# Kernel tuning notes

Hardware: AMD Instinct MI355X
Metric: run time of the kernel (lower is better)

Reference implementation:

```python
import jax, jax.numpy as jnp
import numpy as np

INPUT_SIZE = 1024
HEAD_SIZE = 64


def setup_inputs() -> dict:
    key = jax.random.key(0)
    kx, kk, kq, kv = jax.random.split(key, 4)
    B, T, C, H = 4, 4096, INPUT_SIZE, HEAD_SIZE
    x = jax.random.normal(kx, (B, T, C), dtype=jnp.float32)
    # nn.Linear(C, H, bias=False) weight is (H, C); we store transposed (C, H)
    # so that y = x @ W matches torch's x @ weight.T
    scale = 1.0 / np.sqrt(C)
    Wk = jax.random.uniform(kk, (C, H), dtype=jnp.float32, minval=-scale, maxval=scale)
    Wq = jax.random.uniform(kq, (C, H), dtype=jnp.float32, minval=-scale, maxval=scale)
    Wv = jax.random.uniform(kv, (C, H), dtype=jnp.float32, minval=-scale, maxval=scale)
    return {"x": x, "Wk": Wk, "Wq": Wq, "Wv": Wv}


def reference(x, Wk, Wq, Wv):
    B, T, C = x.shape
    k = x @ Wk  # (B, T, H)
    q = x @ Wq
    v = x @ Wv
    H = k.shape[-1]
    # scaled scores (B, T, T)
    wei = jnp.einsum('bth,bsh->bts', q, k) * (H ** -0.5)
    causal = jnp.tril(jnp.ones((T, T), dtype=bool))
    wei = jnp.where(causal, wei, -jnp.inf)
    wei = jax.nn.softmax(wei, axis=-1)
    out = jnp.einsum('bts,bsh->bth', wei, v)  # (B, T, H)
    return out
```

## Files before the change

kernel.cpp:

```cpp
#include <hip/hip_runtime.h>
#include <math.h>


#define BT   16384
#define TDIM 4096
#define CDIM 1024
#define HDIM 64
#define ACCW 68
#define NSLOT 288

typedef __attribute__((ext_vector_type(8))) short bf16x8;
typedef __attribute__((ext_vector_type(4))) float f32x4;
typedef __attribute__((ext_vector_type(8))) unsigned short us8;
typedef __attribute__((ext_vector_type(4))) unsigned short us4;

static __device__ __forceinline__ unsigned short f2bf(float f) {
    unsigned int u = __float_as_uint(f);
    u += 0x7fffu + ((u >> 16) & 1u);
    return (unsigned short)(u >> 16);
}

static __device__ __forceinline__ void pswap(unsigned &x, unsigned &y) {
    asm("v_permlane32_swap_b32 %0, %1" : "+v"(x), "+v"(y));
    asm("v_permlane16_swap_b32 %0, %1" : "+v"(x), "+v"(y));
}

static __device__ __forceinline__ void softmax_pack(
    const f32x4 sT[4], bool diag, int qloc, int quad,
    bf16x8 &pa0, bf16x8 &pa1)
{
    float p[4][4];
    if (diag) {
        #pragma unroll
        for (int st = 0; st < 4; st++)
            #pragma unroll
            for (int r = 0; r < 4; r++) {
                int kkloc = st * 16 + quad * 4 + r;
                p[st][r] = (kkloc > qloc) ? 0.f : __expf(sT[st][r]);
            }
    } else {
        #pragma unroll
        for (int st = 0; st < 4; st++)
            #pragma unroll
            for (int r = 0; r < 4; r++)
                p[st][r] = __expf(sT[st][r]);
    }
    unsigned cpk[4][2];
    #pragma unroll
    for (int st = 0; st < 4; st++) {
        asm("v_cvt_pk_bf16_f32 %0, %1, %2"
            : "=v"(cpk[st][0]) : "v"(p[st][0]), "v"(p[st][1]));
        asm("v_cvt_pk_bf16_f32 %0, %1, %2"
            : "=v"(cpk[st][1]) : "v"(p[st][2]), "v"(p[st][3]));
    }
    union { unsigned u[4]; bf16x8 v; } u0, u1;
    unsigned a0 = cpk[0][0], b0 = cpk[1][0]; pswap(a0, b0);
    unsigned a1 = cpk[0][1], b1 = cpk[1][1]; pswap(a1, b1);
    u0.u[0] = a0; u0.u[1] = a1; u0.u[2] = b0; u0.u[3] = b1;
    unsigned a2 = cpk[2][0], b2 = cpk[3][0]; pswap(a2, b2);
    unsigned a3 = cpk[2][1], b3 = cpk[3][1]; pswap(a3, b3);
    u1.u[0] = a2; u1.u[1] = a3; u1.u[2] = b2; u1.u[3] = b3;
    pa0 = u0.v; pa1 = u1.v;
}

__global__ __launch_bounds__(256) void wtrans(
    const float* __restrict__ Wk, const float* __restrict__ Wq,
    const float* __restrict__ Wv, unsigned short* __restrict__ wtg)
{
    int idx = blockIdx.x * 256 + threadIdx.x;
    int mat = idx >> 16;
    int rem = idx & 65535;
    int h = rem >> 10, c = rem & 1023;
    const float* W = (mat == 0) ? Wk : (mat == 1) ? Wq : Wv;
    wtg[idx] = f2bf(W[c * HDIM + h]);
}

__global__ __launch_bounds__(512) void qkv_proj(
    const float* __restrict__ x, const unsigned short* __restrict__ wtg,
    unsigned short* __restrict__ kg, unsigned short* __restrict__ qg,
    unsigned short* __restrict__ vtg)
{
    __shared__ __align__(16) unsigned short xs[2][32][72];
    __shared__ __align__(16) unsigned short wts[2][192][72];
    const int t = threadIdx.x;
    const int lane = t & 63, wv = t >> 6, quad = lane >> 4, l16 = lane & 15;
    const int mt = wv >> 2;
    const int nq = wv & 3;
    const int row0 = blockIdx.x * 32;

    const int xr = t >> 4, xc4 = (t & 15) * 4;
    const int wn = t >> 3, wc8 = (t & 7) * 8;

    f32x4 acc3[3];
    #pragma unroll
    for (int i = 0; i < 3; i++) acc3[i] = (f32x4){0.f, 0.f, 0.f, 0.f};

    const size_t xrow = (size_t)(row0 + xr) * CDIM + xc4;

    float4 xq[8];
    #pragma unroll
    for (int c = 0; c < 8; c++)
        xq[c] = *(const float4*)&x[xrow + c * 64];

    us8 w0 = *(const us8*)&wtg[(size_t)(wn +   0) * CDIM + wc8];
    us8 w1 = *(const us8*)&wtg[(size_t)(wn +  64) * CDIM + wc8];
    us8 w2 = *(const us8*)&wtg[(size_t)(wn + 128) * CDIM + wc8];

    {
        us4 pk = { f2bf(xq[0].x), f2bf(xq[0].y), f2bf(xq[0].z), f2bf(xq[0].w) };
        *(us4*)&xs[0][xr][xc4] = pk;
        *(us8*)&wts[0][wn +   0][wc8] = w0;
        *(us8*)&wts[0][wn +  64][wc8] = w1;
        *(us8*)&wts[0][wn + 128][wc8] = w2;
    }
    xq[0] = *(const float4*)&x[xrow + 8 * 64];
    w0 = *(const us8*)&wtg[(size_t)(wn +   0) * CDIM + 64 + wc8];
    w1 = *(const us8*)&wtg[(size_t)(wn +  64) * CDIM + 64 + wc8];
    w2 = *(const us8*)&wtg[(size_t)(wn + 128) * CDIM + 64 + wc8];
    __syncthreads();

    #pragma unroll
    for (int it = 0; it < 16; it++) {
        const int buf = it & 1;
        if (it + 1 < 16) {
            const int sl = (it + 1) & 7;
            us4 pk = { f2bf(xq[sl].x), f2bf(xq[sl].y),
                       f2bf(xq[sl].z), f2bf(xq[sl].w) };
            *(us4*)&xs[buf ^ 1][xr][xc4] = pk;
            *(us8*)&wts[buf ^ 1][wn +   0][wc8] = w0;
            *(us8*)&wts[buf ^ 1][wn +  64][wc8] = w1;
            *(us8*)&wts[buf ^ 1][wn + 128][wc8] = w2;
            if (it + 9 < 16)
                xq[sl] = *(const float4*)&x[xrow + (it + 9) * 64];
            if (it + 2 < 16) {
                int nc = (it + 2) * 64;
                w0 = *(const us8*)&wtg[(size_t)(wn +   0) * CDIM + nc + wc8];
                w1 = *(const us8*)&wtg[(size_t)(wn +  64) * CDIM + nc + wc8];
                w2 = *(const us8*)&wtg[(size_t)(wn + 128) * CDIM + nc + wc8];
            }
        }
        bf16x8 a0 = *(const bf16x8*)&xs[buf][mt * 16 + l16][quad * 8];
        bf16x8 a1 = *(const bf16x8*)&xs[buf][mt * 16 + l16][32 + quad * 8];
        #pragma unroll
        for (int j = 0; j < 3; j++) {
            int nt = nq * 3 + j;
            bf16x8 b0 = *(const bf16x8*)&wts[buf][nt * 16 + l16][quad * 8];
            bf16x8 b1 = *(const bf16x8*)&wts[buf][nt * 16 + l16][32 + quad * 8];
            acc3[j] = __builtin_amdgcn_mfma_f32_16x16x32_bf16(a0, b0, acc3[j], 0, 0, 0);
            acc3[j] = __builtin_amdgcn_mfma_f32_16x16x32_bf16(a1, b1, acc3[j], 0, 0, 0);
        }
        __syncthreads();
    }

    const int mrow = row0 + mt * 16 + quad * 4;
    #pragma unroll
    for (int j = 0; j < 3; j++) {
        int nt = nq * 3 + j;
        int mat = nt >> 2;
        int col = (nt & 3) * 16 + l16;
        if (mat == 2) {
            int bb = mrow >> 12, tr = mrow & 4095;
            us4 pv = { f2bf(acc3[j][0]), f2bf(acc3[j][1]),
                       f2bf(acc3[j][2]), f2bf(acc3[j][3]) };
            *(us4*)&vtg[((size_t)(bb * HDIM + col) << 12) + tr] = pv;
        } else {
            float s = (mat == 1) ? 0.125f : 1.0f;
            unsigned short* dst = (mat == 0) ? kg : qg;
            #pragma unroll
            for (int reg = 0; reg < 4; reg++)
                dst[(size_t)(mrow + reg) * HDIM + col] = f2bf(acc3[j][reg] * s);
        }
    }
}

__global__ __launch_bounds__(256) void attn(
    const unsigned short* __restrict__ qg, const unsigned short* __restrict__ kg,
    const unsigned short* __restrict__ vtg, float* __restrict__ slabs)
{
    __shared__ __align__(16) unsigned short Ks[2][64][72];
    __shared__ __align__(16) unsigned short Vt[2][64][72];

    const int t = threadIdx.x;
    const int lane = t & 63, wv = t >> 6, quad = lane >> 4, l16 = lane & 15;

    const int b = blockIdx.x / NSLOT;
    const int s = blockIdx.x - b * NSLOT;
    int a;
    if      (s < 8)   a = 0;
    else if (s < 24)  a = 1;
    else if (s < 48)  a = 2;
    else if (s < 80)  a = 3;
    else if (s < 120) a = 4;
    else if (s < 168) a = 5;
    else if (s < 224) a = 6;
    else              a = 7;
    const int u  = s - 4 * a * (a + 1);
    const int qt = a * 8 + u / (a + 1);
    const int c  = u % (a + 1);

    const size_t bbase = (size_t)b * TDIM;
    const int Q0 = qt * 64;
    const int kt0 = c * 8;
    const int kt1 = (kt0 + 7 < qt) ? kt0 + 7 : qt;

    const int qrow = Q0 + wv * 16 + l16;
    const bf16x8 qa0 = *(const bf16x8*)&qg[(bbase + qrow) * HDIM + quad * 8];
    const bf16x8 qa1 = *(const bf16x8*)&qg[(bbase + qrow) * HDIM + 32 + quad * 8];

    const short onev = (l16 == 0) ? (short)0x3F80 : (short)0;
    const bf16x8 ones = { onev, onev, onev, onev, onev, onev, onev, onev };

    f32x4 O[5];
    #pragma unroll
    for (int i = 0; i < 5; i++) O[i] = (f32x4){0.f, 0.f, 0.f, 0.f};

    const int fr = t >> 3, fc = (t & 7) * 8;

    us8 kr0 = *(const us8*)&kg[(bbase + kt0 * 64 + fr) * HDIM + fc];
    us8 kr1 = *(const us8*)&kg[(bbase + kt0 * 64 + fr + 32) * HDIM + fc];
    us8 vr0 = *(const us8*)&vtg[((size_t)(b * HDIM + fr) << 12) + kt0 * 64 + fc];
    us8 vr1 = *(const us8*)&vtg[((size_t)(b * HDIM + fr + 32) << 12) + kt0 * 64 + fc];
    *(us8*)&Ks[0][fr][fc] = kr0;
    *(us8*)&Ks[0][fr + 32][fc] = kr1;
    *(us8*)&Vt[0][fr][fc] = vr0;
    *(us8*)&Vt[0][fr + 32][fc] = vr1;
    if (kt0 < kt1) {
        int kn = kt0 + 1;
        kr0 = *(const us8*)&kg[(bbase + kn * 64 + fr) * HDIM + fc];
        kr1 = *(const us8*)&kg[(bbase + kn * 64 + fr + 32) * HDIM + fc];
        vr0 = *(const us8*)&vtg[((size_t)(b * HDIM + fr) << 12) + kn * 64 + fc];
        vr1 = *(const us8*)&vtg[((size_t)(b * HDIM + fr + 32) << 12) + kn * 64 + fc];
    }
    __syncthreads();

    const int qloc = wv * 16 + l16;

    bf16x8 pa0, pa1;
    {
        f32x4 sT[4];
        #pragma unroll
        for (int st = 0; st < 4; st++) {
            bf16x8 kb0 = *(const bf16x8*)&Ks[0][st * 16 + l16][quad * 8];
            bf16x8 kb1 = *(const bf16x8*)&Ks[0][st * 16 + l16][32 + quad * 8];
            f32x4 z = (f32x4){0.f, 0.f, 0.f, 0.f};
            z = __builtin_amdgcn_mfma_f32_16x16x32_bf16(kb0, qa0, z, 0, 0, 0);
            z = __builtin_amdgcn_mfma_f32_16x16x32_bf16(kb1, qa1, z, 0, 0, 0);
            sT[st] = z;
        }
        softmax_pack(sT, kt0 == qt, qloc, quad, pa0, pa1);
    }

    int buf = 0;
    for (int kt = kt0; kt < kt1; ++kt) {
        *(us8*)&Ks[buf ^ 1][fr][fc] = kr0;
        *(us8*)&Ks[buf ^ 1][fr + 32][fc] = kr1;
        *(us8*)&Vt[buf ^ 1][fr][fc] = vr0;
        *(us8*)&Vt[buf ^ 1][fr + 32][fc] = vr1;
        if (kt + 2 <= kt1) {
            int kn = kt + 2;
            kr0 = *(const us8*)&kg[(bbase + kn * 64 + fr) * HDIM + fc];
            kr1 = *(const us8*)&kg[(bbase + kn * 64 + fr + 32) * HDIM + fc];
            vr0 = *(const us8*)&vtg[((size_t)(b * HDIM + fr) << 12) + kn * 64 + fc];
            vr1 = *(const us8*)&vtg[((size_t)(b * HDIM + fr + 32) << 12) + kn * 64 + fc];
        }
        __syncthreads();

        __builtin_amdgcn_s_setprio(1);
        f32x4 sT[4];
        #pragma unroll
        for (int st = 0; st < 4; st++) {
            bf16x8 kb0 = *(const bf16x8*)&Ks[buf ^ 1][st * 16 + l16][quad * 8];
            bf16x8 kb1 = *(const bf16x8*)&Ks[buf ^ 1][st * 16 + l16][32 + quad * 8];
            f32x4 z = (f32x4){0.f, 0.f, 0.f, 0.f};
            z = __builtin_amdgcn_mfma_f32_16x16x32_bf16(kb0, qa0, z, 0, 0, 0);
            z = __builtin_amdgcn_mfma_f32_16x16x32_bf16(kb1, qa1, z, 0, 0, 0);
            sT[st] = z;
        }
        #pragma unroll
        for (int nt = 0; nt < 4; nt++) {
            bf16x8 vb0 = *(const bf16x8*)&Vt[buf][nt * 16 + l16][quad * 8];
            bf16x8 vb1 = *(const bf16x8*)&Vt[buf][nt * 16 + l16][32 + quad * 8];
            O[nt] = __builtin_amdgcn_mfma_f32_16x16x32_bf16(pa0, vb0, O[nt], 0, 0, 0);
            O[nt] = __builtin_amdgcn_mfma_f32_16x16x32_bf16(pa1, vb1, O[nt], 0, 0, 0);
        }
        O[4] = __builtin_amdgcn_mfma_f32_16x16x32_bf16(pa0, ones, O[4], 0, 0, 0);
        O[4] = __builtin_amdgcn_mfma_f32_16x16x32_bf16(pa1, ones, O[4], 0, 0, 0);
        __builtin_amdgcn_s_setprio(0);

        softmax_pack(sT, (kt + 1) == qt, qloc, quad, pa0, pa1);

        __syncthreads();
        buf ^= 1;
    }

    #pragma unroll
    for (int nt = 0; nt < 4; nt++) {
        bf16x8 vb0 = *(const bf16x8*)&Vt[buf][nt * 16 + l16][quad * 8];
        bf16x8 vb1 = *(const bf16x8*)&Vt[buf][nt * 16 + l16][32 + quad * 8];
        O[nt] = __builtin_amdgcn_mfma_f32_16x16x32_bf16(pa0, vb0, O[nt], 0, 0, 0);
        O[nt] = __builtin_amdgcn_mfma_f32_16x16x32_bf16(pa1, vb1, O[nt], 0, 0, 0);
    }
    O[4] = __builtin_amdgcn_mfma_f32_16x16x32_bf16(pa0, ones, O[4], 0, 0, 0);
    O[4] = __builtin_amdgcn_mfma_f32_16x16x32_bf16(pa1, ones, O[4], 0, 0, 0);

    float* slab = slabs + (size_t)(b * NSLOT + s) * 64 * ACCW;
    const int rl = wv * 16 + quad * 4;
    #pragma unroll
    for (int nt = 0; nt < 4; nt++)
        #pragma unroll
        for (int r = 0; r < 4; r++)
            slab[(size_t)(rl + r) * ACCW + nt * 16 + l16] = O[nt][r];
    if (l16 == 0) {
        #pragma unroll
        for (int r = 0; r < 4; r++)
            slab[(size_t)(rl + r) * ACCW + 64] = O[4][r];
    }
}

__global__ __launch_bounds__(256) void reduce_norm(
    const float* __restrict__ slabs, float* __restrict__ out)
{
    int idx = blockIdx.x * 256 + threadIdx.x;
    int row = idx >> 4, c4 = (idx & 15) * 4;
    int b = row >> 12, qt = (row >> 6) & 63, r64 = row & 63;
    int a = qt >> 3, nc = a + 1;
    int base = 4 * a * (a + 1) + (qt & 7) * nc;

    const float* sl = slabs + ((size_t)(b * NSLOT + base) * 64 + r64) * ACCW;
    float4 o = make_float4(0.f, 0.f, 0.f, 0.f);
    float l = 0.f;
    for (int i = 0; i < nc; i++) {
        float4 v = *(const float4*)&sl[c4];
        o.x += v.x; o.y += v.y; o.z += v.z; o.w += v.w;
        l += sl[64];
        sl += (size_t)64 * ACCW;
    }
    float inv = 1.f / l;
    *(float4*)&out[(size_t)row * HDIM + c4] =
        make_float4(o.x * inv, o.y * inv, o.z * inv, o.w * inv);
}

extern "C" void kernel_launch(void* const* d_in, const int* in_sizes, int n_in,
                              void* d_out, int out_size, void* d_ws, size_t ws_size,
                              hipStream_t stream) {
    const float* x  = (const float*)d_in[0];
    const float* Wk = (const float*)d_in[1];
    const float* Wq = (const float*)d_in[2];
    const float* Wv = (const float*)d_in[3];
    float* out = (float*)d_out;

    unsigned short* wtg = (unsigned short*)d_ws;
    unsigned short* kg  = wtg + 196608;
    unsigned short* qg  = kg + (size_t)BT * HDIM;
    unsigned short* vtg = qg + (size_t)BT * HDIM;
    float* slabs = (float*)(vtg + (size_t)4 * HDIM * TDIM);

    wtrans<<<768, 256, 0, stream>>>(Wk, Wq, Wv, wtg);
    qkv_proj<<<BT / 32, 512, 0, stream>>>(x, wtg, kg, qg, vtg);
    attn<<<4 * NSLOT, 256, 0, stream>>>(qg, kg, vtg, slabs);
    reduce_norm<<<BT * HDIM / (4 * 256), 256, 0, stream>>>(slabs, out);
}
```

Before: 138.3 us.

## Split-K the QKV projection across waves and restage attention K/V pipeline

The QKV projection now splits the K dimension of each 64-wide chunk across two wave groups, so each wave computes both 16-row M tiles and reuses one B fragment for two MFMAs. The two partial sums are reduced through shared memory before the epilogue. The attention kernel restructures its double buffering so K tiles are prefetched one step further ahead than V tiles. The K/V shared-memory stores now sit between the QK and PV MFMA phases, which removes one barrier per iteration. The aim is fewer LDS reads in the projection and better overlap of global loads with MFMA work in attention, at the cost of an extra LDS reduction and a more complex buffer-index scheme.

```diff
diff --git a/kernel.cpp b/kernel.cpp
--- a/kernel.cpp
+++ b/kernel.cpp
@@ -84,16 +84,18 @@
     __shared__ __align__(16) unsigned short wts[2][192][72];
     const int t = threadIdx.x;
     const int lane = t & 63, wv = t >> 6, quad = lane >> 4, l16 = lane & 15;
-    const int mt = wv >> 2;
+    const int kh = wv >> 2;
     const int nq = wv & 3;
     const int row0 = blockIdx.x * 32;
 
     const int xr = t >> 4, xc4 = (t & 15) * 4;
     const int wn = t >> 3, wc8 = (t & 7) * 8;
 
-    f32x4 acc3[3];
-    #pragma unroll
-    for (int i = 0; i < 3; i++) acc3[i] = (f32x4){0.f, 0.f, 0.f, 0.f};
+    f32x4 acc[2][3];
+    #pragma unroll
+    for (int m = 0; m < 2; m++)
+        #pragma unroll
+        for (int j = 0; j < 3; j++) acc[m][j] = (f32x4){0.f, 0.f, 0.f, 0.f};
 
     const size_t xrow = (size_t)(row0 + xr) * CDIM + xc4;
 
@@ -139,36 +141,59 @@
                 w2 = *(const us8*)&wtg[(size_t)(wn + 128) * CDIM + nc + wc8];
             }
         }
-        bf16x8 a0 = *(const bf16x8*)&xs[buf][mt * 16 + l16][quad * 8];
-        bf16x8 a1 = *(const bf16x8*)&xs[buf][mt * 16 + l16][32 + quad * 8];
+        bf16x8 a0 = *(const bf16x8*)&xs[buf][l16][kh * 32 + quad * 8];
+        bf16x8 a1 = *(const bf16x8*)&xs[buf][16 + l16][kh * 32 + quad * 8];
         #pragma unroll
         for (int j = 0; j < 3; j++) {
             int nt = nq * 3 + j;
-            bf16x8 b0 = *(const bf16x8*)&wts[buf][nt * 16 + l16][quad * 8];
-            bf16x8 b1 = *(const bf16x8*)&wts[buf][nt * 16 + l16][32 + quad * 8];
-            acc3[j] = __builtin_amdgcn_mfma_f32_16x16x32_bf16(a0, b0, acc3[j], 0, 0, 0);
-            acc3[j] = __builtin_amdgcn_mfma_f32_16x16x32_bf16(a1, b1, acc3[j], 0, 0, 0);
+            bf16x8 bb = *(const bf16x8*)&wts[buf][nt * 16 + l16][kh * 32 + quad * 8];
+            acc[0][j] = __builtin_amdgcn_mfma_f32_16x16x32_bf16(a0, bb, acc[0][j], 0, 0, 0);
+            acc[1][j] = __builtin_amdgcn_mfma_f32_16x16x32_bf16(a1, bb, acc[1][j], 0, 0, 0);
         }
         __syncthreads();
     }
 
-    const int mrow = row0 + mt * 16 + quad * 4;
-    #pragma unroll
-    for (int j = 0; j < 3; j++) {
-        int nt = nq * 3 + j;
-        int mat = nt >> 2;
-        int col = (nt & 3) * 16 + l16;
-        if (mat == 2) {
-            int bb = mrow >> 12, tr = mrow & 4095;
-            us4 pv = { f2bf(acc3[j][0]), f2bf(acc3[j][1]),
-                       f2bf(acc3[j][2]), f2bf(acc3[j][3]) };
-            *(us4*)&vtg[((size_t)(bb * HDIM + col) << 12) + tr] = pv;
-        } else {
-            float s = (mat == 1) ? 0.125f : 1.0f;
-            unsigned short* dst = (mat == 0) ? kg : qg;
+    float* red = (float*)&wts[0][0][0];
+    if (kh == 1) {
+        const int base = ((wv - 4) * 64 + lane) * 24;
+        #pragma unroll
+        for (int m = 0; m < 2; m++)
             #pragma unroll
-            for (int reg = 0; reg < 4; reg++)
-                dst[(size_t)(mrow + reg) * HDIM + col] = f2bf(acc3[j][reg] * s);
+            for (int j = 0; j < 3; j++)
+                *(f32x4*)&red[base + (m * 3 + j) * 4] = acc[m][j];
+    }
+    __syncthreads();
+    if (kh == 0) {
+        const int base = (wv * 64 + lane) * 24;
+        #pragma unroll
+        for (int m = 0; m < 2; m++)
+            #pragma unroll
+            for (int j = 0; j < 3; j++) {
+                f32x4 o = *(const f32x4*)&red[base + (m * 3 + j) * 4];
+                acc[m][j][0] += o[0]; acc[m][j][1] += o[1];
+                acc[m][j][2] += o[2]; acc[m][j][3] += o[3];
+            }
+        #pragma unroll
+        for (int m = 0; m < 2; m++) {
+            const int mrow = row0 + m * 16 + quad * 4;
+            #pragma unroll
+            for (int j = 0; j < 3; j++) {
+                int nt = nq * 3 + j;
+                int mat = nt >> 2;
+                int col = (nt & 3) * 16 + l16;
+                if (mat == 2) {
+                    int bb = mrow >> 12, tr = mrow & 4095;
+                    us4 pv = { f2bf(acc[m][j][0]), f2bf(acc[m][j][1]),
+                               f2bf(acc[m][j][2]), f2bf(acc[m][j][3]) };
+                    *(us4*)&vtg[((size_t)(bb * HDIM + col) << 12) + tr] = pv;
+                } else {
+                    float s = (mat == 1) ? 0.125f : 1.0f;
+                    unsigned short* dst = (mat == 0) ? kg : qg;
+                    #pragma unroll
+                    for (int reg = 0; reg < 4; reg++)
+                        dst[(size_t)(mrow + reg) * HDIM + col] = f2bf(acc[m][j][reg] * s);
+                }
+            }
         }
     }
 }
@@ -215,21 +240,28 @@
     for (int i = 0; i < 5; i++) O[i] = (f32x4){0.f, 0.f, 0.f, 0.f};
 
     const int fr = t >> 3, fc = (t & 7) * 8;
+    const size_t vrow0 = (size_t)(b * HDIM + fr) << 12;
+    const size_t vrow1 = (size_t)(b * HDIM + fr + 32) << 12;
 
     us8 kr0 = *(const us8*)&kg[(bbase + kt0 * 64 + fr) * HDIM + fc];
     us8 kr1 = *(const us8*)&kg[(bbase + kt0 * 64 + fr + 32) * HDIM + fc];
-    us8 vr0 = *(const us8*)&vtg[((size_t)(b * HDIM + fr) << 12) + kt0 * 64 + fc];
-    us8 vr1 = *(const us8*)&vtg[((size_t)(b * HDIM + fr + 32) << 12) + kt0 * 64 + fc];
+    us8 vr0 = *(const us8*)&vtg[vrow0 + kt0 * 64 + fc];
+    us8 vr1 = *(const us8*)&vtg[vrow1 + kt0 * 64 + fc];
     *(us8*)&Ks[0][fr][fc] = kr0;
     *(us8*)&Ks[0][fr + 32][fc] = kr1;
     *(us8*)&Vt[0][fr][fc] = vr0;
     *(us8*)&Vt[0][fr + 32][fc] = vr1;
     if (kt0 < kt1) {
-        int kn = kt0 + 1;
-        kr0 = *(const us8*)&kg[(bbase + kn * 64 + fr) * HDIM + fc];
-        kr1 = *(const us8*)&kg[(bbase + kn * 64 + fr + 32) * HDIM + fc];
-        vr0 = *(const us8*)&vtg[((size_t)(b * HDIM + fr) << 12) + kn * 64 + fc];
-        vr1 = *(const us8*)&vtg[((size_t)(b * HDIM + fr + 32) << 12) + kn * 64 + fc];
+        kr0 = *(const us8*)&kg[(bbase + (kt0 + 1) * 64 + fr) * HDIM + fc];
+        kr1 = *(const us8*)&kg[(bbase + (kt0 + 1) * 64 + fr + 32) * HDIM + fc];
+        *(us8*)&Ks[1][fr][fc] = kr0;
+        *(us8*)&Ks[1][fr + 32][fc] = kr1;
+        vr0 = *(const us8*)&vtg[vrow0 + (kt0 + 1) * 64 + fc];
+        vr1 = *(const us8*)&vtg[vrow1 + (kt0 + 1) * 64 + fc];
+    }
+    if (kt0 + 2 <= kt1) {
+        kr0 = *(const us8*)&kg[(bbase + (kt0 + 2) * 64 + fr) * HDIM + fc];
+        kr1 = *(const us8*)&kg[(bbase + (kt0 + 2) * 64 + fr + 32) * HDIM + fc];
     }
     __syncthreads();
 
@@ -249,37 +281,44 @@
         }
         softmax_pack(sT, kt0 == qt, qloc, quad, pa0, pa1);
     }
-
-    int buf = 0;
+    __syncthreads();
+
     for (int kt = kt0; kt < kt1; ++kt) {
-        *(us8*)&Ks[buf ^ 1][fr][fc] = kr0;
-        *(us8*)&Ks[buf ^ 1][fr + 32][fc] = kr1;
-        *(us8*)&Vt[buf ^ 1][fr][fc] = vr0;
-        *(us8*)&Vt[buf ^ 1][fr + 32][fc] = vr1;
-        if (kt + 2 <= kt1) {
-            int kn = kt + 2;
-            kr0 = *(const us8*)&kg[(bbase + kn * 64 + fr) * HDIM + fc];
-            kr1 = *(const us8*)&kg[(bbase + kn * 64 + fr + 32) * HDIM + fc];
-            vr0 = *(const us8*)&vtg[((size_t)(b * HDIM + fr) << 12) + kn * 64 + fc];
-            vr1 = *(const us8*)&vtg[((size_t)(b * HDIM + fr + 32) << 12) + kn * 64 + fc];
-        }
-        __syncthreads();
+        const int cb = kt & 1;
 
         __builtin_amdgcn_s_setprio(1);
         f32x4 sT[4];
         #pragma unroll
         for (int st = 0; st < 4; st++) {
-            bf16x8 kb0 = *(const bf16x8*)&Ks[buf ^ 1][st * 16 + l16][quad * 8];
-            bf16x8 kb1 = *(const bf16x8*)&Ks[buf ^ 1][st * 16 + l16][32 + quad * 8];
+            bf16x8 kb0 = *(const bf16x8*)&Ks[cb ^ 1][st * 16 + l16][quad * 8];
+            bf16x8 kb1 = *(const bf16x8*)&Ks[cb ^ 1][st * 16 + l16][32 + quad * 8];
             f32x4 z = (f32x4){0.f, 0.f, 0.f, 0.f};
             z = __builtin_amdgcn_mfma_f32_16x16x32_bf16(kb0, qa0, z, 0, 0, 0);
             z = __builtin_amdgcn_mfma_f32_16x16x32_bf16(kb1, qa1, z, 0, 0, 0);
             sT[st] = z;
         }
+        __builtin_amdgcn_s_setprio(0);
+
+        if (kt + 2 <= kt1) {
+            *(us8*)&Ks[cb][fr][fc] = kr0;
+            *(us8*)&Ks[cb][fr + 32][fc] = kr1;
+        }
+        *(us8*)&Vt[cb ^ 1][fr][fc] = vr0;
+        *(us8*)&Vt[cb ^ 1][fr + 32][fc] = vr1;
+        if (kt + 3 <= kt1) {
+            kr0 = *(const us8*)&kg[(bbase + (kt + 3) * 64 + fr) * HDIM + fc];
+            kr1 = *(const us8*)&kg[(bbase + (kt + 3) * 64 + fr + 32) * HDIM + fc];
+        }
+        if (kt + 2 <= kt1) {
+            vr0 = *(const us8*)&vtg[vrow0 + (kt + 2) * 64 + fc];
+            vr1 = *(const us8*)&vtg[vrow1 + (kt + 2) * 64 + fc];
+        }
+
+        __builtin_amdgcn_s_setprio(1);
         #pragma unroll
         for (int nt = 0; nt < 4; nt++) {
-            bf16x8 vb0 = *(const bf16x8*)&Vt[buf][nt * 16 + l16][quad * 8];
-            bf16x8 vb1 = *(const bf16x8*)&Vt[buf][nt * 16 + l16][32 + quad * 8];
+            bf16x8 vb0 = *(const bf16x8*)&Vt[cb][nt * 16 + l16][quad * 8];
+            bf16x8 vb1 = *(const bf16x8*)&Vt[cb][nt * 16 + l16][32 + quad * 8];
             O[nt] = __builtin_amdgcn_mfma_f32_16x16x32_bf16(pa0, vb0, O[nt], 0, 0, 0);
             O[nt] = __builtin_amdgcn_mfma_f32_16x16x32_bf16(pa1, vb1, O[nt], 0, 0, 0);
         }
@@ -290,18 +329,20 @@
         softmax_pack(sT, (kt + 1) == qt, qloc, quad, pa0, pa1);
 
         __syncthreads();
-        buf ^= 1;
-    }
-
-    #pragma unroll
-    for (int nt = 0; nt < 4; nt++) {
-        bf16x8 vb0 = *(const bf16x8*)&Vt[buf][nt * 16 + l16][quad * 8];
-        bf16x8 vb1 = *(const bf16x8*)&Vt[buf][nt * 16 + l16][32 + quad * 8];
-        O[nt] = __builtin_amdgcn_mfma_f32_16x16x32_bf16(pa0, vb0, O[nt], 0, 0, 0);
-        O[nt] = __builtin_amdgcn_mfma_f32_16x16x32_bf16(pa1, vb1, O[nt], 0, 0, 0);
-    }
-    O[4] = __builtin_amdgcn_mfma_f32_16x16x32_bf16(pa0, ones, O[4], 0, 0, 0);
-    O[4] = __builtin_amdgcn_mfma_f32_16x16x32_bf16(pa1, ones, O[4], 0, 0, 0);
+    }
+
+    {
+        const int cb = kt1 & 1;
+        #pragma unroll
+        for (int nt = 0; nt < 4; nt++) {
+            bf16x8 vb0 = *(const bf16x8*)&Vt[cb][nt * 16 + l16][quad * 8];
+            bf16x8 vb1 = *(const bf16x8*)&Vt[cb][nt * 16 + l16][32 + quad * 8];
+            O[nt] = __builtin_amdgcn_mfma_f32_16x16x32_bf16(pa0, vb0, O[nt], 0, 0, 0);
+            O[nt] = __builtin_amdgcn_mfma_f32_16x16x32_bf16(pa1, vb1, O[nt], 0, 0, 0);
+        }
+        O[4] = __builtin_amdgcn_mfma_f32_16x16x32_bf16(pa0, ones, O[4], 0, 0, 0);
+        O[4] = __builtin_amdgcn_mfma_f32_16x16x32_bf16(pa1, ones, O[4], 0, 0, 0);
+    }
 
     float* slab = slabs + (size_t)(b * NSLOT + s) * 64 * ACCW;
     const int rl = wv * 16 + quad * 4;
```

Result: slower. 144.0 us (+4.1%).

## Use direct global-to-LDS loads with XOR swizzle for K/V and weight tiles

Applied to the files above, without the earlier changes.

Replaces register-staged global loads followed by LDS stores with global_load_lds, which writes 16-byte chunks straight into shared memory, in both the projection and attention kernels. Padded LDS rows are replaced by an XOR-swizzled unpadded layout to avoid bank conflicts. The attention K/V double-buffer schedule is restructured around buffer parity, and explicit vmcnt waits are added before barriers. This is meant to cut VGPR pressure and LDS-store instructions, at the cost of waiting on all outstanding loads at each barrier, which may expose load latency.

```diff
diff --git a/kernel.cpp b/kernel.cpp
--- a/kernel.cpp
+++ b/kernel.cpp
@@ -18,6 +18,13 @@
     unsigned int u = __float_as_uint(f);
     u += 0x7fffu + ((u >> 16) & 1u);
     return (unsigned short)(u >> 16);
+}
+
+static __device__ __forceinline__ void gload16(const unsigned short* g,
+                                               unsigned short* l) {
+    __builtin_amdgcn_global_load_lds(
+        (const __attribute__((address_space(1))) void*)g,
+        (__attribute__((address_space(3))) void*)l, 16, 0, 0);
 }
 
 static __device__ __forceinline__ void pswap(unsigned &x, unsigned &y) {
@@ -81,7 +88,7 @@
     unsigned short* __restrict__ vtg)
 {
     __shared__ __align__(16) unsigned short xs[2][32][72];
-    __shared__ __align__(16) unsigned short wts[2][192][72];
+    __shared__ __align__(16) unsigned short wts[2][192][64];
     const int t = threadIdx.x;
     const int lane = t & 63, wv = t >> 6, quad = lane >> 4, l16 = lane & 15;
     const int mt = wv >> 2;
@@ -89,7 +96,11 @@
     const int row0 = blockIdx.x * 32;
 
     const int xr = t >> 4, xc4 = (t & 15) * 4;
-    const int wn = t >> 3, wc8 = (t & 7) * 8;
+    const int gj = lane >> 3, gs = lane & 7;
+    const int sg8 = (gs ^ gj) * 8;
+    const int h3 = l16 & 15 & 7;
+    const int sA = (quad ^ h3) * 8;
+    const int sB = ((quad + 4) ^ h3) * 8;
 
     f32x4 acc3[3];
     #pragma unroll
@@ -97,58 +108,47 @@
 
     const size_t xrow = (size_t)(row0 + xr) * CDIM + xc4;
 
-    float4 xq[8];
-    #pragma unroll
-    for (int c = 0; c < 8; c++)
-        xq[c] = *(const float4*)&x[xrow + c * 64];
-
-    us8 w0 = *(const us8*)&wtg[(size_t)(wn +   0) * CDIM + wc8];
-    us8 w1 = *(const us8*)&wtg[(size_t)(wn +  64) * CDIM + wc8];
-    us8 w2 = *(const us8*)&wtg[(size_t)(wn + 128) * CDIM + wc8];
-
+    float4 xv = *(const float4*)&x[xrow];
+    #pragma unroll
+    for (int j = 0; j < 3; j++) {
+        int r = wv * 24 + j * 8 + gj;
+        gload16(&wtg[(size_t)r * CDIM + sg8], &wts[0][wv * 24 + j * 8][0]);
+    }
     {
-        us4 pk = { f2bf(xq[0].x), f2bf(xq[0].y), f2bf(xq[0].z), f2bf(xq[0].w) };
+        us4 pk = { f2bf(xv.x), f2bf(xv.y), f2bf(xv.z), f2bf(xv.w) };
         *(us4*)&xs[0][xr][xc4] = pk;
-        *(us8*)&wts[0][wn +   0][wc8] = w0;
-        *(us8*)&wts[0][wn +  64][wc8] = w1;
-        *(us8*)&wts[0][wn + 128][wc8] = w2;
-    }
-    xq[0] = *(const float4*)&x[xrow + 8 * 64];
-    w0 = *(const us8*)&wtg[(size_t)(wn +   0) * CDIM + 64 + wc8];
-    w1 = *(const us8*)&wtg[(size_t)(wn +  64) * CDIM + 64 + wc8];
-    w2 = *(const us8*)&wtg[(size_t)(wn + 128) * CDIM + 64 + wc8];
+    }
+    float4 xvp = *(const float4*)&x[xrow + 64];
+    asm volatile("s_waitcnt vmcnt(0)" ::: "memory");
     __syncthreads();
 
     #pragma unroll
     for (int it = 0; it < 16; it++) {
         const int buf = it & 1;
         if (it + 1 < 16) {
-            const int sl = (it + 1) & 7;
-            us4 pk = { f2bf(xq[sl].x), f2bf(xq[sl].y),
-                       f2bf(xq[sl].z), f2bf(xq[sl].w) };
+            const int nc = (it + 1) * 64;
+            #pragma unroll
+            for (int j = 0; j < 3; j++) {
+                int r = wv * 24 + j * 8 + gj;
+                gload16(&wtg[(size_t)r * CDIM + nc + sg8],
+                        &wts[buf ^ 1][wv * 24 + j * 8][0]);
+            }
+            us4 pk = { f2bf(xvp.x), f2bf(xvp.y), f2bf(xvp.z), f2bf(xvp.w) };
             *(us4*)&xs[buf ^ 1][xr][xc4] = pk;
-            *(us8*)&wts[buf ^ 1][wn +   0][wc8] = w0;
-            *(us8*)&wts[buf ^ 1][wn +  64][wc8] = w1;
-            *(us8*)&wts[buf ^ 1][wn + 128][wc8] = w2;
-            if (it + 9 < 16)
-                xq[sl] = *(const float4*)&x[xrow + (it + 9) * 64];
-            if (it + 2 < 16) {
-                int nc = (it + 2) * 64;
-                w0 = *(const us8*)&wtg[(size_t)(wn +   0) * CDIM + nc + wc8];
-                w1 = *(const us8*)&wtg[(size_t)(wn +  64) * CDIM + nc + wc8];
-                w2 = *(const us8*)&wtg[(size_t)(wn + 128) * CDIM + nc + wc8];
-            }
+            if (it + 2 < 16)
+                xvp = *(const float4*)&x[xrow + (it + 2) * 64];
         }
         bf16x8 a0 = *(const bf16x8*)&xs[buf][mt * 16 + l16][quad * 8];
         bf16x8 a1 = *(const bf16x8*)&xs[buf][mt * 16 + l16][32 + quad * 8];
         #pragma unroll
         for (int j = 0; j < 3; j++) {
             int nt = nq * 3 + j;
-            bf16x8 b0 = *(const bf16x8*)&wts[buf][nt * 16 + l16][quad * 8];
-            bf16x8 b1 = *(const bf16x8*)&wts[buf][nt * 16 + l16][32 + quad * 8];
+            bf16x8 b0 = *(const bf16x8*)&wts[buf][nt * 16 + l16][sA];
+            bf16x8 b1 = *(const bf16x8*)&wts[buf][nt * 16 + l16][sB];
             acc3[j] = __builtin_amdgcn_mfma_f32_16x16x32_bf16(a0, b0, acc3[j], 0, 0, 0);
             acc3[j] = __builtin_amdgcn_mfma_f32_16x16x32_bf16(a1, b1, acc3[j], 0, 0, 0);
         }
+        asm volatile("s_waitcnt vmcnt(0)" ::: "memory");
         __syncthreads();
     }
 
@@ -177,8 +177,8 @@
     const unsigned short* __restrict__ qg, const unsigned short* __restrict__ kg,
     const unsigned short* __restrict__ vtg, float* __restrict__ slabs)
 {
-    __shared__ __align__(16) unsigned short Ks[2][64][72];
-    __shared__ __align__(16) unsigned short Vt[2][64][72];
+    __shared__ __align__(16) unsigned short Ks[2][64][64];
+    __shared__ __align__(16) unsigned short Vt[2][64][64];
 
     const int t = threadIdx.x;
     const int lane = t & 63, wv = t >> 6, quad = lane >> 4, l16 = lane & 15;
@@ -203,6 +203,12 @@
     const int kt0 = c * 8;
     const int kt1 = (kt0 + 7 < qt) ? kt0 + 7 : qt;
 
+    const int gj = lane >> 3, gs = lane & 7;
+    const int sg8 = (gs ^ gj) * 8;
+    const int h3 = l16 & 7;
+    const int sA = (quad ^ h3) * 8;
+    const int sB = ((quad + 4) ^ h3) * 8;
+
     const int qrow = Q0 + wv * 16 + l16;
     const bf16x8 qa0 = *(const bf16x8*)&qg[(bbase + qrow) * HDIM + quad * 8];
     const bf16x8 qa1 = *(const bf16x8*)&qg[(bbase + qrow) * HDIM + 32 + quad * 8];
@@ -214,23 +220,23 @@
     #pragma unroll
     for (int i = 0; i < 5; i++) O[i] = (f32x4){0.f, 0.f, 0.f, 0.f};
 
-    const int fr = t >> 3, fc = (t & 7) * 8;
-
-    us8 kr0 = *(const us8*)&kg[(bbase + kt0 * 64 + fr) * HDIM + fc];
-    us8 kr1 = *(const us8*)&kg[(bbase + kt0 * 64 + fr + 32) * HDIM + fc];
-    us8 vr0 = *(const us8*)&vtg[((size_t)(b * HDIM + fr) << 12) + kt0 * 64 + fc];
-    us8 vr1 = *(const us8*)&vtg[((size_t)(b * HDIM + fr + 32) << 12) + kt0 * 64 + fc];
-    *(us8*)&Ks[0][fr][fc] = kr0;
-    *(us8*)&Ks[0][fr + 32][fc] = kr1;
-    *(us8*)&Vt[0][fr][fc] = vr0;
-    *(us8*)&Vt[0][fr + 32][fc] = vr1;
+    #pragma unroll
+    for (int j = 0; j < 2; j++) {
+        const int r = wv * 16 + j * 8 + gj;
+        gload16(&kg[(bbase + kt0 * 64 + r) * HDIM + sg8],
+                &Ks[kt0 & 1][wv * 16 + j * 8][0]);
+        gload16(&vtg[((size_t)(b * HDIM + r) << 12) + kt0 * 64 + sg8],
+                &Vt[kt0 & 1][wv * 16 + j * 8][0]);
+    }
     if (kt0 < kt1) {
-        int kn = kt0 + 1;
-        kr0 = *(const us8*)&kg[(bbase + kn * 64 + fr) * HDIM + fc];
-        kr1 = *(const us8*)&kg[(bbase + kn * 64 + fr + 32) * HDIM + fc];
-        vr0 = *(const us8*)&vtg[((size_t)(b * HDIM + fr) << 12) + kn * 64 + fc];
-        vr1 = *(const us8*)&vtg[((size_t)(b * HDIM + fr + 32) << 12) + kn * 64 + fc];
-    }
+        #pragma unroll
+        for (int j = 0; j < 2; j++) {
+            const int r = wv * 16 + j * 8 + gj;
+            gload16(&kg[(bbase + (kt0 + 1) * 64 + r) * HDIM + sg8],
+                    &Ks[(kt0 + 1) & 1][wv * 16 + j * 8][0]);
+        }
+    }
+    asm volatile("s_waitcnt vmcnt(0)" ::: "memory");
     __syncthreads();
 
     const int qloc = wv * 16 + l16;
@@ -240,8 +246,8 @@
         f32x4 sT[4];
         #pragma unroll
         for (int st = 0; st < 4; st++) {
-            bf16x8 kb0 = *(const bf16x8*)&Ks[0][st * 16 + l16][quad * 8];
-            bf16x8 kb1 = *(const bf16x8*)&Ks[0][st * 16 + l16][32 + quad * 8];
+            bf16x8 kb0 = *(const bf16x8*)&Ks[kt0 & 1][st * 16 + l16][sA];
+            bf16x8 kb1 = *(const bf16x8*)&Ks[kt0 & 1][st * 16 + l16][sB];
             f32x4 z = (f32x4){0.f, 0.f, 0.f, 0.f};
             z = __builtin_amdgcn_mfma_f32_16x16x32_bf16(kb0, qa0, z, 0, 0, 0);
             z = __builtin_amdgcn_mfma_f32_16x16x32_bf16(kb1, qa1, z, 0, 0, 0);
@@ -249,28 +255,32 @@
         }
         softmax_pack(sT, kt0 == qt, qloc, quad, pa0, pa1);
     }
-
-    int buf = 0;
+    __syncthreads();
+
     for (int kt = kt0; kt < kt1; ++kt) {
-        *(us8*)&Ks[buf ^ 1][fr][fc] = kr0;
-        *(us8*)&Ks[buf ^ 1][fr + 32][fc] = kr1;
-        *(us8*)&Vt[buf ^ 1][fr][fc] = vr0;
-        *(us8*)&Vt[buf ^ 1][fr + 32][fc] = vr1;
+        const int cb = kt & 1;
+
         if (kt + 2 <= kt1) {
-            int kn = kt + 2;
-            kr0 = *(const us8*)&kg[(bbase + kn * 64 + fr) * HDIM + fc];
-            kr1 = *(const us8*)&kg[(bbase + kn * 64 + fr + 32) * HDIM + fc];
-            vr0 = *(const us8*)&vtg[((size_t)(b * HDIM + fr) << 12) + kn * 64 + fc];
-            vr1 = *(const us8*)&vtg[((size_t)(b * HDIM + fr + 32) << 12) + kn * 64 + fc];
-        }
-        __syncthreads();
+            #pragma unroll
+            for (int j = 0; j < 2; j++) {
+                const int r = wv * 16 + j * 8 + gj;
+                gload16(&kg[(bbase + (kt + 2) * 64 + r) * HDIM + sg8],
+                        &Ks[cb][wv * 16 + j * 8][0]);
+            }
+        }
+        #pragma unroll
+        for (int j = 0; j < 2; j++) {
+            const int r = wv * 16 + j * 8 + gj;
+            gload16(&vtg[((size_t)(b * HDIM + r) << 12) + (kt + 1) * 64 + sg8],
+                    &Vt[cb ^ 1][wv * 16 + j * 8][0]);
+        }
 
         __builtin_amdgcn_s_setprio(1);
         f32x4 sT[4];
         #pragma unroll
         for (int st = 0; st < 4; st++) {
-            bf16x8 kb0 = *(const bf16x8*)&Ks[buf ^ 1][st * 16 + l16][quad * 8];
-            bf16x8 kb1 = *(const bf16x8*)&Ks[buf ^ 1][st * 16 + l16][32 + quad * 8];
+            bf16x8 kb0 = *(const bf16x8*)&Ks[cb ^ 1][st * 16 + l16][sA];
+            bf16x8 kb1 = *(const bf16x8*)&Ks[cb ^ 1][st * 16 + l16][sB];
             f32x4 z = (f32x4){0.f, 0.f, 0.f, 0.f};
             z = __builtin_amdgcn_mfma_f32_16x16x32_bf16(kb0, qa0, z, 0, 0, 0);
             z = __builtin_amdgcn_mfma_f32_16x16x32_bf16(kb1, qa1, z, 0, 0, 0);
@@ -278,8 +288,8 @@
         }
         #pragma unroll
         for (int nt = 0; nt < 4; nt++) {
-            bf16x8 vb0 = *(const bf16x8*)&Vt[buf][nt * 16 + l16][quad * 8];
-            bf16x8 vb1 = *(const bf16x8*)&Vt[buf][nt * 16 + l16][32 + quad * 8];
+            bf16x8 vb0 = *(const bf16x8*)&Vt[cb][nt * 16 + l16][sA];
+            bf16x8 vb1 = *(const bf16x8*)&Vt[cb][nt * 16 + l16][sB];
             O[nt] = __builtin_amdgcn_mfma_f32_16x16x32_bf16(pa0, vb0, O[nt], 0, 0, 0);
             O[nt] = __builtin_amdgcn_mfma_f32_16x16x32_bf16(pa1, vb1, O[nt], 0, 0, 0);
         }
@@ -289,19 +299,22 @@
 
         softmax_pack(sT, (kt + 1) == qt, qloc, quad, pa0, pa1);
 
+        asm volatile("s_waitcnt vmcnt(0)" ::: "memory");
         __syncthreads();
-        buf ^= 1;
-    }
-
-    #pragma unroll
-    for (int nt = 0; nt < 4; nt++) {
-        bf16x8 vb0 = *(const bf16x8*)&Vt[buf][nt * 16 + l16][quad * 8];
-        bf16x8 vb1 = *(const bf16x8*)&Vt[buf][nt * 16 + l16][32 + quad * 8];
-        O[nt] = __builtin_amdgcn_mfma_f32_16x16x32_bf16(pa0, vb0, O[nt], 0, 0, 0);
-        O[nt] = __builtin_amdgcn_mfma_f32_16x16x32_bf16(pa1, vb1, O[nt], 0, 0, 0);
-    }
-    O[4] = __builtin_amdgcn_mfma_f32_16x16x32_bf16(pa0, ones, O[4], 0, 0, 0);
-    O[4] = __builtin_amdgcn_mfma_f32_16x16x32_bf16(pa1, ones, O[4], 0, 0, 0);
+    }
+
+    {
+        const int cb = kt1 & 1;
+        #pragma unroll
+        for (int nt = 0; nt < 4; nt++) {
+            bf16x8 vb0 = *(const bf16x8*)&Vt[cb][nt * 16 + l16][sA];
+            bf16x8 vb1 = *(const bf16x8*)&Vt[cb][nt * 16 + l16][sB];
+            O[nt] = __builtin_amdgcn_mfma_f32_16x16x32_bf16(pa0, vb0, O[nt], 0, 0, 0);
+            O[nt] = __builtin_amdgcn_mfma_f32_16x16x32_bf16(pa1, vb1, O[nt], 0, 0, 0);
+        }
+        O[4] = __builtin_amdgcn_mfma_f32_16x16x32_bf16(pa0, ones, O[4], 0, 0, 0);
+        O[4] = __builtin_amdgcn_mfma_f32_16x16x32_bf16(pa1, ones, O[4], 0, 0, 0);
+    }
 
     float* slab = slabs + (size_t)(b * NSLOT + s) * 64 * ACCW;
     const int rl = wv * 16 + quad * 4;
```

After: 140.3 us. No clear change (+1.4%).

## Widen attention blocks to 128 query rows sharing each K/V tile

Applied to the files above, without the earlier changes.

Each attention block now covers 128 query rows (two 64-row query tiles, 8 waves, 512 threads) instead of 64, so every K/V tile staged in shared memory is reused by twice as many waves. Global-to-LDS loads per thread drop to one K and one V vector per tile. Waves in the lower query tile skip QK and PV work on the diagonal tile beyond their causal limit, and blocks are launched in reverse order so the longest-running ones start first. The slab layout and reduce kernel are re-indexed for the new split. The cost is half as many blocks, which lowers parallelism, and some waves sit idle while the others finish the diagonal tile.

```diff
diff --git a/kernel.cpp b/kernel.cpp
--- a/kernel.cpp
+++ b/kernel.cpp
@@ -7,7 +7,7 @@
 #define CDIM 1024
 #define HDIM 64
 #define ACCW 68
-#define NSLOT 288
+#define NSLOT 144
 
 typedef __attribute__((ext_vector_type(8))) short bf16x8;
 typedef __attribute__((ext_vector_type(4))) float f32x4;
@@ -173,7 +173,7 @@
     }
 }
 
-__global__ __launch_bounds__(256) void attn(
+__global__ __launch_bounds__(512) void attn(
     const unsigned short* __restrict__ qg, const unsigned short* __restrict__ kg,
     const unsigned short* __restrict__ vtg, float* __restrict__ slabs)
 {
@@ -184,24 +184,28 @@
     const int lane = t & 63, wv = t >> 6, quad = lane >> 4, l16 = lane & 15;
 
     const int b = blockIdx.x / NSLOT;
-    const int s = blockIdx.x - b * NSLOT;
-    int a;
-    if      (s < 8)   a = 0;
-    else if (s < 24)  a = 1;
-    else if (s < 48)  a = 2;
-    else if (s < 80)  a = 3;
-    else if (s < 120) a = 4;
-    else if (s < 168) a = 5;
-    else if (s < 224) a = 6;
-    else              a = 7;
-    const int u  = s - 4 * a * (a + 1);
-    const int qt = a * 8 + u / (a + 1);
-    const int c  = u % (a + 1);
+    const int s = NSLOT - 1 - (blockIdx.x - b * NSLOT);
+    int g;
+    if      (s < 4)   g = 0;
+    else if (s < 12)  g = 1;
+    else if (s < 24)  g = 2;
+    else if (s < 40)  g = 3;
+    else if (s < 60)  g = 4;
+    else if (s < 84)  g = 5;
+    else if (s < 112) g = 6;
+    else              g = 7;
+    const int u = s - 2 * g * (g + 1);
+    const int i = 4 * g + u / (g + 1);
+    const int c = u % (g + 1);
 
     const size_t bbase = (size_t)b * TDIM;
-    const int Q0 = qt * 64;
+    const int Q0 = i * 128;
     const int kt0 = c * 8;
-    const int kt1 = (kt0 + 7 < qt) ? kt0 + 7 : qt;
+    const int kt1 = (kt0 + 7 < 2 * i + 1) ? kt0 + 7 : 2 * i + 1;
+
+    const int wg = wv >> 2;
+    const int myqt = 2 * i + wg;
+    const int mykt1 = (kt1 < myqt) ? kt1 : myqt;
 
     const int qrow = Q0 + wv * 16 + l16;
     const bf16x8 qa0 = *(const bf16x8*)&qg[(bbase + qrow) * HDIM + quad * 8];
@@ -212,28 +216,22 @@
 
     f32x4 O[5];
     #pragma unroll
-    for (int i = 0; i < 5; i++) O[i] = (f32x4){0.f, 0.f, 0.f, 0.f};
+    for (int n = 0; n < 5; n++) O[n] = (f32x4){0.f, 0.f, 0.f, 0.f};
 
     const int fr = t >> 3, fc = (t & 7) * 8;
 
-    us8 kr0 = *(const us8*)&kg[(bbase + kt0 * 64 + fr) * HDIM + fc];
-    us8 kr1 = *(const us8*)&kg[(bbase + kt0 * 64 + fr + 32) * HDIM + fc];
-    us8 vr0 = *(const us8*)&vtg[((size_t)(b * HDIM + fr) << 12) + kt0 * 64 + fc];
-    us8 vr1 = *(const us8*)&vtg[((size_t)(b * HDIM + fr + 32) << 12) + kt0 * 64 + fc];
-    *(us8*)&Ks[0][fr][fc] = kr0;
-    *(us8*)&Ks[0][fr + 32][fc] = kr1;
-    *(us8*)&Vt[0][fr][fc] = vr0;
-    *(us8*)&Vt[0][fr + 32][fc] = vr1;
+    us8 kr = *(const us8*)&kg[(bbase + kt0 * 64 + fr) * HDIM + fc];
+    us8 vr = *(const us8*)&vtg[((size_t)(b * HDIM + fr) << 12) + kt0 * 64 + fc];
+    *(us8*)&Ks[0][fr][fc] = kr;
+    *(us8*)&Vt[0][fr][fc] = vr;
     if (kt0 < kt1) {
         int kn = kt0 + 1;
-        kr0 = *(const us8*)&kg[(bbase + kn * 64 + fr) * HDIM + fc];
-        kr1 = *(const us8*)&kg[(bbase + kn * 64 + fr + 32) * HDIM + fc];
-        vr0 = *(const us8*)&vtg[((size_t)(b * HDIM + fr) << 12) + kn * 64 + fc];
-        vr1 = *(const us8*)&vtg[((size_t)(b * HDIM + fr + 32) << 12) + kn * 64 + fc];
+        kr = *(const us8*)&kg[(bbase + kn * 64 + fr) * HDIM + fc];
+        vr = *(const us8*)&vtg[((size_t)(b * HDIM + fr) << 12) + kn * 64 + fc];
     }
     __syncthreads();
 
-    const int qloc = wv * 16 + l16;
+    const int qloc = (wv & 3) * 16 + l16;
 
     bf16x8 pa0, pa1;
     {
@@ -247,34 +245,34 @@
             z = __builtin_amdgcn_mfma_f32_16x16x32_bf16(kb1, qa1, z, 0, 0, 0);
             sT[st] = z;
         }
-        softmax_pack(sT, kt0 == qt, qloc, quad, pa0, pa1);
+        softmax_pack(sT, kt0 == myqt, qloc, quad, pa0, pa1);
     }
 
     int buf = 0;
     for (int kt = kt0; kt < kt1; ++kt) {
-        *(us8*)&Ks[buf ^ 1][fr][fc] = kr0;
-        *(us8*)&Ks[buf ^ 1][fr + 32][fc] = kr1;
-        *(us8*)&Vt[buf ^ 1][fr][fc] = vr0;
-        *(us8*)&Vt[buf ^ 1][fr + 32][fc] = vr1;
+        *(us8*)&Ks[buf ^ 1][fr][fc] = kr;
+        *(us8*)&Vt[buf ^ 1][fr][fc] = vr;
         if (kt + 2 <= kt1) {
             int kn = kt + 2;
-            kr0 = *(const us8*)&kg[(bbase + kn * 64 + fr) * HDIM + fc];
-            kr1 = *(const us8*)&kg[(bbase + kn * 64 + fr + 32) * HDIM + fc];
-            vr0 = *(const us8*)&vtg[((size_t)(b * HDIM + fr) << 12) + kn * 64 + fc];
-            vr1 = *(const us8*)&vtg[((size_t)(b * HDIM + fr + 32) << 12) + kn * 64 + fc];
+            kr = *(const us8*)&kg[(bbase + kn * 64 + fr) * HDIM + fc];
+            vr = *(const us8*)&vtg[((size_t)(b * HDIM + fr) << 12) + kn * 64 + fc];
         }
         __syncthreads();
+
+        const bool nextQK = (kt + 1 <= mykt1);
 
         __builtin_amdgcn_s_setprio(1);
         f32x4 sT[4];
-        #pragma unroll
-        for (int st = 0; st < 4; st++) {
-            bf16x8 kb0 = *(const bf16x8*)&Ks[buf ^ 1][st * 16 + l16][quad * 8];
-            bf16x8 kb1 = *(const bf16x8*)&Ks[buf ^ 1][st * 16 + l16][32 + quad * 8];
-            f32x4 z = (f32x4){0.f, 0.f, 0.f, 0.f};
-            z = __builtin_amdgcn_mfma_f32_16x16x32_bf16(kb0, qa0, z, 0, 0, 0);
-            z = __builtin_amdgcn_mfma_f32_16x16x32_bf16(kb1, qa1, z, 0, 0, 0);
-            sT[st] = z;
+        if (nextQK) {
+            #pragma unroll
+            for (int st = 0; st < 4; st++) {
+                bf16x8 kb0 = *(const bf16x8*)&Ks[buf ^ 1][st * 16 + l16][quad * 8];
+                bf16x8 kb1 = *(const bf16x8*)&Ks[buf ^ 1][st * 16 + l16][32 + quad * 8];
+                f32x4 z = (f32x4){0.f, 0.f, 0.f, 0.f};
+                z = __builtin_amdgcn_mfma_f32_16x16x32_bf16(kb0, qa0, z, 0, 0, 0);
+                z = __builtin_amdgcn_mfma_f32_16x16x32_bf16(kb1, qa1, z, 0, 0, 0);
+                sT[st] = z;
+            }
         }
         #pragma unroll
         for (int nt = 0; nt < 4; nt++) {
@@ -287,23 +285,26 @@
         O[4] = __builtin_amdgcn_mfma_f32_16x16x32_bf16(pa1, ones, O[4], 0, 0, 0);
         __builtin_amdgcn_s_setprio(0);
 
-        softmax_pack(sT, (kt + 1) == qt, qloc, quad, pa0, pa1);
+        if (nextQK)
+            softmax_pack(sT, (kt + 1) == myqt, qloc, quad, pa0, pa1);
 
         __syncthreads();
         buf ^= 1;
     }
 
-    #pragma unroll
-    for (int nt = 0; nt < 4; nt++) {
-        bf16x8 vb0 = *(const bf16x8*)&Vt[buf][nt * 16 + l16][quad * 8];
-        bf16x8 vb1 = *(const bf16x8*)&Vt[buf][nt * 16 + l16][32 + quad * 8];
-        O[nt] = __builtin_amdgcn_mfma_f32_16x16x32_bf16(pa0, vb0, O[nt], 0, 0, 0);
-        O[nt] = __builtin_amdgcn_mfma_f32_16x16x32_bf16(pa1, vb1, O[nt], 0, 0, 0);
-    }
-    O[4] = __builtin_amdgcn_mfma_f32_16x16x32_bf16(pa0, ones, O[4], 0, 0, 0);
-    O[4] = __builtin_amdgcn_mfma_f32_16x16x32_bf16(pa1, ones, O[4], 0, 0, 0);
-
-    float* slab = slabs + (size_t)(b * NSLOT + s) * 64 * ACCW;
+    if (kt1 <= mykt1) {
+        #pragma unroll
+        for (int nt = 0; nt < 4; nt++) {
+            bf16x8 vb0 = *(const bf16x8*)&Vt[buf][nt * 16 + l16][quad * 8];
+            bf16x8 vb1 = *(const bf16x8*)&Vt[buf][nt * 16 + l16][32 + quad * 8];
+            O[nt] = __builtin_amdgcn_mfma_f32_16x16x32_bf16(pa0, vb0, O[nt], 0, 0, 0);
+            O[nt] = __builtin_amdgcn_mfma_f32_16x16x32_bf16(pa1, vb1, O[nt], 0, 0, 0);
+        }
+        O[4] = __builtin_amdgcn_mfma_f32_16x16x32_bf16(pa0, ones, O[4], 0, 0, 0);
+        O[4] = __builtin_amdgcn_mfma_f32_16x16x32_bf16(pa1, ones, O[4], 0, 0, 0);
+    }
+
+    float* slab = slabs + (size_t)(b * NSLOT + s) * 128 * ACCW;
     const int rl = wv * 16 + quad * 4;
     #pragma unroll
     for (int nt = 0; nt < 4; nt++)
@@ -322,18 +323,18 @@
 {
     int idx = blockIdx.x * 256 + threadIdx.x;
     int row = idx >> 4, c4 = (idx & 15) * 4;
-    int b = row >> 12, qt = (row >> 6) & 63, r64 = row & 63;
-    int a = qt >> 3, nc = a + 1;
-    int base = 4 * a * (a + 1) + (qt & 7) * nc;
-
-    const float* sl = slabs + ((size_t)(b * NSLOT + base) * 64 + r64) * ACCW;
+    int b = row >> 12, i = (row >> 7) & 31, r128 = row & 127;
+    int g = i >> 2, nc = g + 1;
+    int base = 2 * g * (g + 1) + (i & 3) * nc;
+
+    const float* sl = slabs + ((size_t)(b * NSLOT + base) * 128 + r128) * ACCW;
     float4 o = make_float4(0.f, 0.f, 0.f, 0.f);
     float l = 0.f;
-    for (int i = 0; i < nc; i++) {
+    for (int k = 0; k < nc; k++) {
         float4 v = *(const float4*)&sl[c4];
         o.x += v.x; o.y += v.y; o.z += v.z; o.w += v.w;
         l += sl[64];
-        sl += (size_t)64 * ACCW;
+        sl += (size_t)128 * ACCW;
     }
     float inv = 1.f / l;
     *(float4*)&out[(size_t)row * HDIM + c4] =
@@ -357,6 +358,6 @@
 
     wtrans<<<768, 256, 0, stream>>>(Wk, Wq, Wv, wtg);
     qkv_proj<<<BT / 32, 512, 0, stream>>>(x, wtg, kg, qg, vtg);
-    attn<<<4 * NSLOT, 256, 0, stream>>>(qg, kg, vtg, slabs);
+    attn<<<4 * NSLOT, 512, 0, stream>>>(qg, kg, vtg, slabs);
     reduce_norm<<<BT * HDIM / (4 * 256), 256, 0, stream>>>(slabs, out);
 }
```

Result: slower. 141.6 us (+2.3%).
